# Performance work log

Hardware: AMD Instinct MI355X
Metric: run time of the kernel (lower is better)

## Reference

```python
import jax, jax.numpy as jnp
import numpy as np

B, T, H = 32, 2048, 1024

def setup_inputs() -> dict:
    key = jax.random.key(0)
    k1, k2, k3 = jax.random.split(key, 3)
    gru_output = jax.random.normal(k1, (B, T, H), dtype=jnp.float32)
    # Xavier uniform bounds
    lim_w = float(np.sqrt(6.0 / (H + H)))
    lim_c = float(np.sqrt(6.0 / (H + 1)))
    attention_weights = jax.random.uniform(k2, (H, H), minval=-lim_w, maxval=lim_w, dtype=jnp.float32)
    context_vector = jax.random.uniform(k3, (H, 1), minval=-lim_c, maxval=lim_c, dtype=jnp.float32)
    return {"gru_output": gru_output, "attention_weights": attention_weights, "context_vector": context_vector}

def reference(gru_output, attention_weights, context_vector):
    # score: [B, T, H]
    score = jnp.tanh(jnp.einsum('bth,hk->btk', gru_output, attention_weights))
    # logits: [B, T]
    logits = jnp.einsum('bth,h->bt', score, context_vector[:, 0])
    attn = jax.nn.softmax(logits, axis=1)  # over time dim
    # context: [B, H]
    context = jnp.einsum('bth,bt->bh', gru_output, attn)
    return (context, attn)
```

## Files before the change

kernel.cpp:

```cpp
#include <hip/hip_runtime.h>
#include <hip/hip_bf16.h>
#include <stdint.h>

#define B_DIM 32
#define T_DIM 2048
#define H_DIM 1024
#define M_DIM (B_DIM * T_DIM)
#define K_DIM H_DIM
#define N_DIM H_DIM

#define BM 256
#define BN 256
#define BKT 32
#define NTILES (K_DIM / BKT)
#define DEPTH 3

typedef __attribute__((ext_vector_type(4))) float f32x4;
typedef __attribute__((ext_vector_type(8))) short short8;
typedef __attribute__((ext_vector_type(4))) short short4v;

__device__ __forceinline__ unsigned short f2bf(float x) {
  unsigned u = __float_as_uint(x);
  return (unsigned short)((u + 0x7FFFu + ((u >> 16) & 1u)) >> 16);
}
__device__ __forceinline__ float bf2f(unsigned short h) {
  return __uint_as_float(((unsigned)h) << 16);
}
__device__ __forceinline__ float fast_tanh(float x) {
  float e = __expf(2.f * x);
  return 1.f - 2.f / (e + 1.f);
}
__device__ __forceinline__ int swz(int r, int s) {
  return ((r >> 1) << 7) + (((((r & 1) << 2) | s) ^ ((r >> 1) & 7)) << 4);
}

__global__ void convert_g_kernel(const float* __restrict__ in,
                                 unsigned short* __restrict__ out) {
  size_t nvec = (size_t)M_DIM * K_DIM / 8;
  size_t stride = (size_t)gridDim.x * blockDim.x;
  for (size_t i = (size_t)blockIdx.x * blockDim.x + threadIdx.x; i < nvec;
       i += stride) {
    const float4* p = (const float4*)(in + i * 8);
    float4 u0 = p[0], u1 = p[1];
    short8 s;
    s[0] = (short)f2bf(u0.x); s[1] = (short)f2bf(u0.y);
    s[2] = (short)f2bf(u0.z); s[3] = (short)f2bf(u0.w);
    s[4] = (short)f2bf(u1.x); s[5] = (short)f2bf(u1.y);
    s[6] = (short)f2bf(u1.z); s[7] = (short)f2bf(u1.w);
    *(short8*)(out + i * 8) = s;
  }
}

__global__ void convert_w_kernel(const float* __restrict__ w,
                                 unsigned short* __restrict__ wt) {
  __shared__ float tile[64][65];
  int n0 = blockIdx.x * 64;
  int k0 = blockIdx.y * 64;
  int j = threadIdx.x & 63;
  int i0 = threadIdx.x >> 6;
#pragma unroll
  for (int ii = 0; ii < 16; ++ii) {
    int i = i0 * 16 + ii;
    tile[i][j] = w[(size_t)(k0 + i) * H_DIM + n0 + j];
  }
  __syncthreads();
#pragma unroll
  for (int ii = 0; ii < 16; ++ii) {
    int i = i0 * 16 + ii;
    wt[(size_t)(n0 + i) * H_DIM + k0 + j] = f2bf(tile[j][i]);
  }
}

__global__ __launch_bounds__(512, 2) void gemm_tanh_logits(
    const unsigned short* __restrict__ A,
    const unsigned short* __restrict__ Bt,
    const float* __restrict__ cvec,
    float* __restrict__ logits) {
  __shared__ unsigned short lds[4][BM * BKT + BN * BKT];

  const int tid = threadIdx.x;
  const int wid = tid >> 6;
  const int lane = tid & 63;

  int p = blockIdx.x;
  int logical = (p & 7) * 128 + (p >> 3);
  int mrow = logical >> 2;
  int ncol = logical & 3;

  const unsigned short* Ap = A + (size_t)mrow * BM * K_DIM;
  const unsigned short* Bp = Bt + (size_t)ncol * BN * K_DIM;

  auto stage_half = [&](int t, int h) {
    int buf = t & 3;
    const unsigned short* gp = h ? Bp : Ap;
    unsigned short* base = &lds[buf][h ? BM * BKT : 0];
#pragma unroll
    for (int j = 0; j < 2; ++j) {
      int o = j * 8192 + tid * 16;
      int pr = o >> 7;
      int v = ((o >> 4) & 7) ^ (pr & 7);
      int r = (pr << 1) | (v >> 2);
      int s = v & 3;
      const unsigned short* ga = gp + (size_t)r * K_DIM + t * BKT + s * 8;
      unsigned short* la = base + ((j * 8192 + wid * 1024) >> 1);
      __builtin_amdgcn_global_load_lds(
          (const __attribute__((address_space(1))) unsigned int*)ga,
          (__attribute__((address_space(3))) unsigned int*)la, 16, 0, 0);
    }
  };

  const int wm = wid >> 2;
  const int wn = wid & 3;
  const int fr = lane & 15;
  const int sl = lane >> 4;

  const int aoff = swz(wm * 128 + fr, sl) >> 1;
  const int boff = (swz(wn * 64 + fr, sl) >> 1) + BM * BKT;

  f32x4 acc[8][4];
#pragma unroll
  for (int m = 0; m < 8; ++m)
#pragma unroll
    for (int n = 0; n < 4; ++n) acc[m][n] = (f32x4){0.f, 0.f, 0.f, 0.f};

  stage_half(0, 0); stage_half(0, 1);
  stage_half(1, 0); stage_half(1, 1);
  stage_half(2, 0); stage_half(2, 1);
  asm volatile("s_waitcnt vmcnt(8)" ::: "memory");
  __builtin_amdgcn_s_barrier();

  for (int t = 0; t < NTILES; ++t) {
    const unsigned short* L0 = &lds[t & 3][0];
    short8 a[4], b[4];
    asm volatile("" ::: "memory");
    if (t + DEPTH < NTILES) stage_half(t + DEPTH, 0);
#pragma unroll
    for (int m = 0; m < 4; ++m) a[m] = *(const short8*)(L0 + aoff + m * 512);
#pragma unroll
    for (int n = 0; n < 4; ++n) b[n] = *(const short8*)(L0 + boff + n * 512);
    __builtin_amdgcn_s_setprio(1);
#pragma unroll
    for (int m = 0; m < 4; ++m)
#pragma unroll
      for (int n = 0; n < 4; ++n)
        acc[m][n] = __builtin_amdgcn_mfma_f32_16x16x32_bf16(a[m], b[n],
                                                            acc[m][n], 0, 0, 0);
    __builtin_amdgcn_s_setprio(0);
    asm volatile("" ::: "memory");
    __builtin_amdgcn_s_barrier();
    asm volatile("" ::: "memory");
    if (t + DEPTH < NTILES) stage_half(t + DEPTH, 1);
#pragma unroll
    for (int m = 0; m < 4; ++m)
      a[m] = *(const short8*)(L0 + aoff + (m + 4) * 512);
    __builtin_amdgcn_s_setprio(1);
#pragma unroll
    for (int m = 0; m < 4; ++m)
#pragma unroll
      for (int n = 0; n < 4; ++n)
        acc[m + 4][n] = __builtin_amdgcn_mfma_f32_16x16x32_bf16(
            a[m], b[n], acc[m + 4][n], 0, 0, 0);
    __builtin_amdgcn_s_setprio(0);
    asm volatile("" ::: "memory");
    if (t < NTILES - DEPTH)
      asm volatile("s_waitcnt vmcnt(8)" ::: "memory");
    else if (t == NTILES - DEPTH)
      asm volatile("s_waitcnt vmcnt(4)" ::: "memory");
    else if (t == NTILES - 2)
      asm volatile("s_waitcnt vmcnt(0)" ::: "memory");
    __builtin_amdgcn_s_barrier();
  }

  const int cgrp = lane >> 4;
  const int cidx = lane & 15;
  const int colb = ncol * BN + wn * 64;
  const int rowb = mrow * BM + wm * 128;
#pragma unroll
  for (int m = 0; m < 8; ++m) {
    float s0 = 0.f, s1 = 0.f, s2 = 0.f, s3 = 0.f;
#pragma unroll
    for (int n = 0; n < 4; ++n) {
      float cw = cvec[colb + n * 16 + cidx];
      s0 += fast_tanh(acc[m][n][0]) * cw;
      s1 += fast_tanh(acc[m][n][1]) * cw;
      s2 += fast_tanh(acc[m][n][2]) * cw;
      s3 += fast_tanh(acc[m][n][3]) * cw;
    }
#pragma unroll
    for (int mask = 1; mask < 16; mask <<= 1) {
      s0 += __shfl_xor(s0, mask);
      s1 += __shfl_xor(s1, mask);
      s2 += __shfl_xor(s2, mask);
      s3 += __shfl_xor(s3, mask);
    }
    if (cidx == 0) {
      int row = rowb + m * 16 + cgrp * 4;
      atomicAdd(&logits[row + 0], s0);
      atomicAdd(&logits[row + 1], s1);
      atomicAdd(&logits[row + 2], s2);
      atomicAdd(&logits[row + 3], s3);
    }
  }
}

__global__ void softmax_kernel(float* __restrict__ la) {
  int b = blockIdx.x;
  float* row = la + (size_t)b * T_DIM;
  int tid = threadIdx.x;
  int wid = tid >> 6, lane = tid & 63;
  __shared__ float red[4];

  float v[8];
  float mx = -3.4e38f;
#pragma unroll
  for (int i = 0; i < 8; ++i) {
    v[i] = row[tid + i * 256];
    mx = fmaxf(mx, v[i]);
  }
#pragma unroll
  for (int mask = 32; mask >= 1; mask >>= 1) mx = fmaxf(mx, __shfl_xor(mx, mask));
  if (lane == 0) red[wid] = mx;
  __syncthreads();
  mx = fmaxf(fmaxf(red[0], red[1]), fmaxf(red[2], red[3]));
  __syncthreads();

  float sum = 0.f;
#pragma unroll
  for (int i = 0; i < 8; ++i) {
    v[i] = __expf(v[i] - mx);
    sum += v[i];
  }
#pragma unroll
  for (int mask = 32; mask >= 1; mask >>= 1) sum += __shfl_xor(sum, mask);
  if (lane == 0) red[wid] = sum;
  __syncthreads();
  sum = red[0] + red[1] + red[2] + red[3];
  float inv = 1.f / sum;
#pragma unroll
  for (int i = 0; i < 8; ++i) row[tid + i * 256] = v[i] * inv;
}

__global__ void context_kernel(const unsigned short* __restrict__ Gb,
                               const float* __restrict__ attn,
                               float* __restrict__ ctx) {
  int tc = blockIdx.x;
  int b = blockIdx.y;
  int h = threadIdx.x * 4;
  const unsigned short* g = Gb + ((size_t)b * T_DIM + tc * 128) * H_DIM + h;
  const float* a = attn + b * T_DIM + tc * 128;
  float s0 = 0.f, s1 = 0.f, s2 = 0.f, s3 = 0.f;
#pragma unroll 4
  for (int t = 0; t < 128; ++t) {
    short4v v = *(const short4v*)(g + (size_t)t * H_DIM);
    float w = a[t];
    s0 += w * bf2f((unsigned short)v[0]);
    s1 += w * bf2f((unsigned short)v[1]);
    s2 += w * bf2f((unsigned short)v[2]);
    s3 += w * bf2f((unsigned short)v[3]);
  }
  float* cb = ctx + b * H_DIM + h;
  atomicAdd(cb + 0, s0);
  atomicAdd(cb + 1, s1);
  atomicAdd(cb + 2, s2);
  atomicAdd(cb + 3, s3);
}

extern "C" void kernel_launch(void* const* d_in, const int* in_sizes, int n_in,
                              void* d_out, int out_size, void* d_ws, size_t ws_size,
                              hipStream_t stream) {
  const float* G = (const float*)d_in[0];
  const float* W = (const float*)d_in[1];
  const float* c = (const float*)d_in[2];
  float* out = (float*)d_out;
  float* ctx = out;
  float* attn = out + B_DIM * H_DIM;

  unsigned short* Gb = (unsigned short*)d_ws;
  unsigned short* Wt = (unsigned short*)((char*)d_ws +
                                         (size_t)M_DIM * K_DIM * 2);

  hipMemsetAsync(d_out, 0, (size_t)out_size * sizeof(float), stream);

  convert_g_kernel<<<4096, 256, 0, stream>>>(G, Gb);
  convert_w_kernel<<<dim3(16, 16), 256, 0, stream>>>(W, Wt);
  gemm_tanh_logits<<<1024, 512, 0, stream>>>(Gb, Wt, c, attn);
  softmax_kernel<<<B_DIM, 256, 0, stream>>>(attn);
  context_kernel<<<dim3(16, 32), 256, 0, stream>>>(Gb, attn, ctx);
}
```

Measured before the change: 571.6 us.

## Unroll GEMM main loop by four with precomputed staging addresses and explicit schedule barriers

Precomputes per-thread global source pointers and LDS destinations once, so the loop no longer recomputes the swizzle address math on every stage. The K loop is unrolled by four so buffer indices become compile-time constants. LDS fragment reads are now issued before the async global-to-LDS stages and fenced with sched_barrier, s_barrier and lgkmcnt waits, forcing a fixed interleave of loads and MFMA. This adds extra barriers per tile, which may cost more than the scheduling it gains. The epilogue also hoists the context-vector loads out of the row loop.

```diff
diff --git a/kernel.cpp b/kernel.cpp
--- a/kernel.cpp
+++ b/kernel.cpp
@@ -76,7 +76,7 @@
     const unsigned short* __restrict__ Bt,
     const float* __restrict__ cvec,
     float* __restrict__ logits) {
-  __shared__ unsigned short lds[4][BM * BKT + BN * BKT];
+  __shared__ unsigned short lds[4 * 16384];
 
   const int tid = threadIdx.x;
   const int wid = tid >> 6;
@@ -90,23 +90,39 @@
   const unsigned short* Ap = A + (size_t)mrow * BM * K_DIM;
   const unsigned short* Bp = Bt + (size_t)ncol * BN * K_DIM;
 
-  auto stage_half = [&](int t, int h) {
-    int buf = t & 3;
-    const unsigned short* gp = h ? Bp : Ap;
-    unsigned short* base = &lds[buf][h ? BM * BKT : 0];
-#pragma unroll
-    for (int j = 0; j < 2; ++j) {
-      int o = j * 8192 + tid * 16;
-      int pr = o >> 7;
-      int v = ((o >> 4) & 7) ^ (pr & 7);
-      int r = (pr << 1) | (v >> 2);
-      int s = v & 3;
-      const unsigned short* ga = gp + (size_t)r * K_DIM + t * BKT + s * 8;
-      unsigned short* la = base + ((j * 8192 + wid * 1024) >> 1);
-      __builtin_amdgcn_global_load_lds(
-          (const __attribute__((address_space(1))) unsigned int*)ga,
-          (__attribute__((address_space(3))) unsigned int*)la, 16, 0, 0);
-    }
+  const unsigned short *gA[2], *gB[2];
+#pragma unroll
+  for (int j = 0; j < 2; ++j) {
+    int o = j * 8192 + tid * 16;
+    int pr = o >> 7;
+    int v = ((o >> 4) & 7) ^ (pr & 7);
+    int r = (pr << 1) | (v >> 2);
+    int s = v & 3;
+    gA[j] = Ap + (size_t)r * K_DIM + s * 8;
+    gB[j] = Bp + (size_t)r * K_DIM + s * 8;
+  }
+  const int ldst0 = wid * 512;
+  const int ldst1 = wid * 512 + 4096;
+
+  auto stageA = [&](int tt, int bi) {
+    __builtin_amdgcn_global_load_lds(
+        (const __attribute__((address_space(1))) unsigned int*)(gA[0] + tt * BKT),
+        (__attribute__((address_space(3))) unsigned int*)(lds + bi * 16384 + ldst0),
+        16, 0, 0);
+    __builtin_amdgcn_global_load_lds(
+        (const __attribute__((address_space(1))) unsigned int*)(gA[1] + tt * BKT),
+        (__attribute__((address_space(3))) unsigned int*)(lds + bi * 16384 + ldst1),
+        16, 0, 0);
+  };
+  auto stageB = [&](int tt, int bi) {
+    __builtin_amdgcn_global_load_lds(
+        (const __attribute__((address_space(1))) unsigned int*)(gB[0] + tt * BKT),
+        (__attribute__((address_space(3))) unsigned int*)(lds + bi * 16384 + 8192 + ldst0),
+        16, 0, 0);
+    __builtin_amdgcn_global_load_lds(
+        (const __attribute__((address_space(1))) unsigned int*)(gB[1] + tt * BKT),
+        (__attribute__((address_space(3))) unsigned int*)(lds + bi * 16384 + 8192 + ldst1),
+        16, 0, 0);
   };
 
   const int wm = wid >> 2;
@@ -115,7 +131,7 @@
   const int sl = lane >> 4;
 
   const int aoff = swz(wm * 128 + fr, sl) >> 1;
-  const int boff = (swz(wn * 64 + fr, sl) >> 1) + BM * BKT;
+  const int boff = (swz(wn * 64 + fr, sl) >> 1) + 8192;
 
   f32x4 acc[8][4];
 #pragma unroll
@@ -123,68 +139,80 @@
 #pragma unroll
     for (int n = 0; n < 4; ++n) acc[m][n] = (f32x4){0.f, 0.f, 0.f, 0.f};
 
-  stage_half(0, 0); stage_half(0, 1);
-  stage_half(1, 0); stage_half(1, 1);
-  stage_half(2, 0); stage_half(2, 1);
+  stageA(0, 0); stageB(0, 0);
+  stageA(1, 1); stageB(1, 1);
+  stageA(2, 2); stageB(2, 2);
   asm volatile("s_waitcnt vmcnt(8)" ::: "memory");
   __builtin_amdgcn_s_barrier();
 
-  for (int t = 0; t < NTILES; ++t) {
-    const unsigned short* L0 = &lds[t & 3][0];
-    short8 a[4], b[4];
-    asm volatile("" ::: "memory");
-    if (t + DEPTH < NTILES) stage_half(t + DEPTH, 0);
-#pragma unroll
-    for (int m = 0; m < 4; ++m) a[m] = *(const short8*)(L0 + aoff + m * 512);
-#pragma unroll
-    for (int n = 0; n < 4; ++n) b[n] = *(const short8*)(L0 + boff + n * 512);
-    __builtin_amdgcn_s_setprio(1);
-#pragma unroll
-    for (int m = 0; m < 4; ++m)
-#pragma unroll
-      for (int n = 0; n < 4; ++n)
-        acc[m][n] = __builtin_amdgcn_mfma_f32_16x16x32_bf16(a[m], b[n],
-                                                            acc[m][n], 0, 0, 0);
-    __builtin_amdgcn_s_setprio(0);
-    asm volatile("" ::: "memory");
-    __builtin_amdgcn_s_barrier();
-    asm volatile("" ::: "memory");
-    if (t + DEPTH < NTILES) stage_half(t + DEPTH, 1);
-#pragma unroll
-    for (int m = 0; m < 4; ++m)
-      a[m] = *(const short8*)(L0 + aoff + (m + 4) * 512);
-    __builtin_amdgcn_s_setprio(1);
-#pragma unroll
-    for (int m = 0; m < 4; ++m)
-#pragma unroll
-      for (int n = 0; n < 4; ++n)
-        acc[m + 4][n] = __builtin_amdgcn_mfma_f32_16x16x32_bf16(
-            a[m], b[n], acc[m + 4][n], 0, 0, 0);
-    __builtin_amdgcn_s_setprio(0);
-    asm volatile("" ::: "memory");
-    if (t < NTILES - DEPTH)
-      asm volatile("s_waitcnt vmcnt(8)" ::: "memory");
-    else if (t == NTILES - DEPTH)
-      asm volatile("s_waitcnt vmcnt(4)" ::: "memory");
-    else if (t == NTILES - 2)
-      asm volatile("s_waitcnt vmcnt(0)" ::: "memory");
-    __builtin_amdgcn_s_barrier();
+  for (int T = 0; T < NTILES; T += 4) {
+#pragma unroll
+    for (int u = 0; u < 4; ++u) {
+      const int t = T + u;
+      const unsigned short* L0 = lds + u * 16384;
+      short8 a[4], b[4], a2[4];
+#pragma unroll
+      for (int m = 0; m < 4; ++m) a[m] = *(const short8*)(L0 + aoff + m * 512);
+#pragma unroll
+      for (int n = 0; n < 4; ++n) b[n] = *(const short8*)(L0 + boff + n * 512);
+      if (t + DEPTH < NTILES) stageA(t + DEPTH, (u + 3) & 3);
+      __builtin_amdgcn_sched_barrier(0);
+      __builtin_amdgcn_s_barrier();
+      asm volatile("s_waitcnt lgkmcnt(0)" ::: "memory");
+      __builtin_amdgcn_sched_barrier(0);
+      __builtin_amdgcn_s_setprio(1);
+#pragma unroll
+      for (int m = 0; m < 4; ++m)
+#pragma unroll
+        for (int n = 0; n < 4; ++n)
+          acc[m][n] = __builtin_amdgcn_mfma_f32_16x16x32_bf16(a[m], b[n],
+                                                              acc[m][n], 0, 0, 0);
+      __builtin_amdgcn_s_setprio(0);
+      __builtin_amdgcn_sched_barrier(0);
+      __builtin_amdgcn_s_barrier();
+#pragma unroll
+      for (int m = 0; m < 4; ++m)
+        a2[m] = *(const short8*)(L0 + aoff + (m + 4) * 512);
+      if (t + DEPTH < NTILES) stageB(t + DEPTH, (u + 3) & 3);
+      __builtin_amdgcn_sched_barrier(0);
+      __builtin_amdgcn_s_barrier();
+      asm volatile("s_waitcnt lgkmcnt(0)" ::: "memory");
+      __builtin_amdgcn_sched_barrier(0);
+      __builtin_amdgcn_s_setprio(1);
+#pragma unroll
+      for (int m = 0; m < 4; ++m)
+#pragma unroll
+        for (int n = 0; n < 4; ++n)
+          acc[m + 4][n] = __builtin_amdgcn_mfma_f32_16x16x32_bf16(
+              a2[m], b[n], acc[m + 4][n], 0, 0, 0);
+      __builtin_amdgcn_s_setprio(0);
+      __builtin_amdgcn_sched_barrier(0);
+      if (t < NTILES - DEPTH)
+        asm volatile("s_waitcnt vmcnt(8)" ::: "memory");
+      else if (t == NTILES - DEPTH)
+        asm volatile("s_waitcnt vmcnt(4)" ::: "memory");
+      else if (t == NTILES - 2)
+        asm volatile("s_waitcnt vmcnt(0)" ::: "memory");
+      __builtin_amdgcn_s_barrier();
+    }
   }
 
   const int cgrp = lane >> 4;
   const int cidx = lane & 15;
   const int colb = ncol * BN + wn * 64;
   const int rowb = mrow * BM + wm * 128;
+  float cw[4];
+#pragma unroll
+  for (int n = 0; n < 4; ++n) cw[n] = cvec[colb + n * 16 + cidx];
 #pragma unroll
   for (int m = 0; m < 8; ++m) {
     float s0 = 0.f, s1 = 0.f, s2 = 0.f, s3 = 0.f;
 #pragma unroll
     for (int n = 0; n < 4; ++n) {
-      float cw = cvec[colb + n * 16 + cidx];
-      s0 += fast_tanh(acc[m][n][0]) * cw;
-      s1 += fast_tanh(acc[m][n][1]) * cw;
-      s2 += fast_tanh(acc[m][n][2]) * cw;
-      s3 += fast_tanh(acc[m][n][3]) * cw;
+      s0 += fast_tanh(acc[m][n][0]) * cw[n];
+      s1 += fast_tanh(acc[m][n][1]) * cw[n];
+      s2 += fast_tanh(acc[m][n][2]) * cw[n];
+      s3 += fast_tanh(acc[m][n][3]) * cw[n];
     }
 #pragma unroll
     for (int mask = 1; mask < 16; mask <<= 1) {
```

Result: no change. 565.8 us (-1.0%).
